# Performance work log

Hardware: AMD Instinct MI355X
Metric: run time of the kernel (lower is better)

## Reference

```python
import jax, jax.numpy as jnp
import numpy as np

N, E, FN, FE, L, G = 4096, 16384, 16, 8, 128, 64
EPS = 1e-5


def setup_inputs() -> dict:
    key = jax.random.key(0)
    ks = iter(jax.random.split(key, 40))

    def lin_w(shape):
        return jax.random.normal(next(ks), shape, jnp.float32) * (1.0 / np.sqrt(shape[0]))

    d = {}
    d["x"] = jax.random.normal(next(ks), (N, FN), jnp.float32)
    d["edge_attr"] = jax.random.normal(next(ks), (E, FE), jnp.float32)
    d["edge_index"] = jax.random.randint(next(ks), (2, E), 0, N)
    d["batch"] = jnp.sort(jax.random.randint(next(ks), (N,), 0, G))
    for i, (cin, cout) in enumerate([(FN, 32), (32, 64), (64, 128)], 1):
        d[f"We{i}"] = lin_w((FE, cin * cout))          # edge_fc weight
        d[f"be{i}"] = jnp.zeros((cin * cout,), jnp.float32)
        d[f"bias{i}"] = jnp.zeros((cout,), jnp.float32)
        d[f"Wr{i}"] = lin_w((cin, cout))               # res_fc weight
        d[f"br{i}"] = jnp.zeros((cout,), jnp.float32)
        d[f"bn_g{i}"] = jnp.ones((cout,), jnp.float32)
        d[f"bn_b{i}"] = jnp.zeros((cout,), jnp.float32)
        d[f"a{i}"] = jnp.float32(0.25)                  # PReLU slope
    d["Wi"] = lin_w((128, 128)); d["bi"] = jnp.zeros((128,), jnp.float32)
    d["Wj"] = lin_w((128, 128)); d["bj"] = jnp.zeros((128,), jnp.float32)
    d["Wfc"] = lin_w((128, 2 * L)); d["bfc"] = jnp.zeros((2 * L,), jnp.float32)
    return d


def _ecc(x, src, dst, norm, edge_attr, We, be, bias, Wr, br, cout, cin):
    # dynamically generated per-edge filter: [E, out, in]
    theta = (edge_attr @ We + be).reshape(E, cout, cin)
    # gather source features, per-edge matvec, degree-normalize (norm_j)
    msg = norm[src][:, None] * jnp.einsum('eoi,ei->eo', theta, x[src])
    # scatter-add into destination nodes + bias + residual linear
    return jax.ops.segment_sum(msg, dst, num_segments=N) + bias + x @ Wr + br


def _bn(x, g, b):
    m = x.mean(0)
    v = x.var(0)  # biased variance, as torch BN training normalization
    return (x - m) * jax.lax.rsqrt(v + EPS) * g + b


def _prelu(x, a):
    return jnp.where(x >= 0, x, a * x)


def reference(x, edge_attr, edge_index, batch,
              We1, be1, bias1, Wr1, br1, bn_g1, bn_b1, a1,
              We2, be2, bias2, Wr2, br2, bn_g2, bn_b2, a2,
              We3, be3, bias3, Wr3, br3, bn_g3, bn_b3, a3,
              Wi, bi, Wj, bj, Wfc, bfc):
    src, dst = edge_index[0], edge_index[1]
    deg = jax.ops.segment_sum(jnp.ones((E,), x.dtype), src, num_segments=N)
    norm = jnp.where(deg > 0, 1.0 / deg, 0.0)

    h = _ecc(x, src, dst, norm, edge_attr, We1, be1, bias1, Wr1, br1, 32, FN)
    h = _prelu(_bn(h, bn_g1, bn_b1), a1)
    h = _ecc(h, src, dst, norm, edge_attr, We2, be2, bias2, Wr2, br2, 64, 32)
    h = _prelu(_bn(h, bn_g2, bn_b2), a2)
    h = _ecc(h, src, dst, norm, edge_attr, We3, be3, bias3, Wr3, br3, 128, 64)
    h = _prelu(_bn(h, bn_g3, bn_b3), a3)

    # gated attention pooling (GGS-NN eq. 7), scatter-sum per graph
    gates = jax.nn.sigmoid(h @ Wi + bi)
    feats = jnp.tanh(h @ Wj + bj)
    pooled = jnp.tanh(jax.ops.segment_sum(gates * feats, batch, num_segments=G))

    z = pooled @ Wfc + bfc  # [G, 2L]
    return z[:, :L], z[:, L:]
```

## Files before the change

### kernel.cpp

```cpp
#include <hip/hip_runtime.h>
#include <math.h>

#define NN 4096
#define NE 16384
#define NG 64

#define OFF_DEG   0
#define OFF_H1    4096
#define OFF_H2    135168
#define OFF_H3    397312
#define OFF_ST1   921600
#define OFF_ST2   921664
#define OFF_ST3   921792
#define OFF_POOL  922048
#define OFF_WC1   930240
#define OFF_WC2   934848
#define OFF_WC3   953280
#define OFF_Y     1027008
#define ZERO_FLOATS 930240

__device__ __forceinline__ void tr_wcat(const float* We, const float* be,
                                        float* Wcat, int CIN, int COUT, int t) {
    int nine = 9 * COUT;
    int i = t / nine; int r = t - i * nine;
    int f = r / COUT; int o = r - f * COUT;
    Wcat[t] = (f < 8) ? We[f * CIN * COUT + o * CIN + i] : be[o * CIN + i];
}

__global__ __launch_bounds__(256) void k_prep(
    const float* __restrict__ We1, const float* __restrict__ be1,
    const float* __restrict__ We2, const float* __restrict__ be2,
    const float* __restrict__ We3, const float* __restrict__ be3,
    const int* __restrict__ ei, float* __restrict__ ws)
{
    int t = blockIdx.x * 256 + threadIdx.x;
    if (t < 4608)  { tr_wcat(We1, be1, ws + OFF_WC1, 16, 32, t); return; }
    t -= 4608;
    if (t < 18432) { tr_wcat(We2, be2, ws + OFF_WC2, 32, 64, t); return; }
    t -= 18432;
    if (t < 73728) { tr_wcat(We3, be3, ws + OFF_WC3, 64, 128, t); return; }
    t -= 73728;
    if (t < NE)    { atomicAdd(&ws[OFF_DEG + ei[t]], 1.0f); }
}

template<int K>
__global__ __launch_bounds__(256) void k_proj(
    const float* __restrict__ A,
    const float* __restrict__ B,
    const float* __restrict__ deg,
    float* __restrict__ Y, int Ncols)
{
    __shared__ float sA[K][68];
    __shared__ float sB[K][68];
    const int tid = threadIdx.x;
    const int m0 = blockIdx.x * 64;
    const int n0 = blockIdx.y * 64;

    for (int t = tid; t < 64 * K; t += 256) {
        int m = t / K, i = t - m * K;
        sA[i][m] = A[(m0 + m) * K + i];
    }
    for (int t = tid; t < 64 * K; t += 256) {
        int i = t / 64, n = t - i * 64;
        int col = n0 + n;
        sB[i][n] = (col < Ncols) ? B[i * Ncols + col] : 0.f;
    }
    __syncthreads();

    const int tn = tid % 16, tm = tid / 16;
    float acc[4][4] = {{0.f}};
#pragma unroll 8
    for (int i = 0; i < K; ++i) {
        float4 a = *(const float4*)&sA[i][tm * 4];
        float4 b = *(const float4*)&sB[i][tn * 4];
        acc[0][0] += a.x * b.x; acc[0][1] += a.x * b.y; acc[0][2] += a.x * b.z; acc[0][3] += a.x * b.w;
        acc[1][0] += a.y * b.x; acc[1][1] += a.y * b.y; acc[1][2] += a.y * b.z; acc[1][3] += a.y * b.w;
        acc[2][0] += a.z * b.x; acc[2][1] += a.z * b.y; acc[2][2] += a.z * b.z; acc[2][3] += a.z * b.w;
        acc[3][0] += a.w * b.x; acc[3][1] += a.w * b.y; acc[3][2] += a.w * b.z; acc[3][3] += a.w * b.w;
    }

#pragma unroll
    for (int mm = 0; mm < 4; ++mm) {
        int m = m0 + tm * 4 + mm;
        float d = deg[m];
        float nrm = d > 0.f ? 1.f / d : 0.f;
#pragma unroll
        for (int nn = 0; nn < 4; ++nn) {
            int col = n0 + tn * 4 + nn;
            if (col < Ncols) Y[(size_t)m * Ncols + col] = acc[mm][nn] * nrm;
        }
    }
}

template<int COUT>
__global__ __launch_bounds__(256) void k_egather(
    const float* __restrict__ Y, const float* __restrict__ eattr,
    const int* __restrict__ ei, float* __restrict__ h)
{
    int idx = blockIdx.x * 256 + threadIdx.x;
    int e = idx / COUT;
    int o = idx - e * COUT;
    int src = ei[e], dst = ei[NE + e];
    const float* y = Y + (size_t)src * (9 * COUT);
    const float* ea = eattr + e * 8;
    float acc = y[8 * COUT + o];
#pragma unroll
    for (int f = 0; f < 8; ++f) acc += ea[f] * y[f * COUT + o];
    atomicAdd(&h[dst * COUT + o], acc);
}

template<int CIN, int COUT, int KN>
__global__ __launch_bounds__(256) void k_node(
    const float* __restrict__ xin, const float* __restrict__ Wr,
    const float* __restrict__ br, const float* __restrict__ bias,
    float* __restrict__ h, float* __restrict__ st)
{
    constexpr int NL = 256 / COUT;
    constexpr int NB = NL * KN;
    constexpr int CINP = CIN | 1;
    __shared__ float sWr[CIN * COUT];
    __shared__ float sX[NB * CINP];
    __shared__ float sred[256];
    const int tid = threadIdx.x;
    const int nbase = blockIdx.x * NB;

    for (int t = tid; t < CIN * COUT; t += 256) sWr[t] = Wr[t];
    for (int t = tid; t < NB * CIN; t += 256) {
        int r = t / CIN, i = t - r * CIN;
        sX[r * CINP + i] = xin[(nbase + r) * CIN + i];
    }
    __syncthreads();

    const int o = tid % COUT;
    const int nl = tid / COUT;
    const float addc = bias[o] + br[o];
    float sum = 0.f, sumsq = 0.f;
    for (int k = 0; k < KN; ++k) {
        int r = nl * KN + k;
        float a = addc;
        for (int i = 0; i < CIN; ++i)
            a += sX[r * CINP + i] * sWr[i * COUT + o];
        int gi = (nbase + r) * COUT + o;
        float hv = h[gi] + a;
        h[gi] = hv;
        sum += hv; sumsq += hv * hv;
    }
    sred[tid] = sum;
    __syncthreads();
    if (tid < COUT) {
        float s = 0.f;
        for (int g2 = 0; g2 < NL; ++g2) s += sred[g2 * COUT + tid];
        atomicAdd(&st[tid], s);
    }
    __syncthreads();
    sred[tid] = sumsq;
    __syncthreads();
    if (tid < COUT) {
        float s = 0.f;
        for (int g2 = 0; g2 < NL; ++g2) s += sred[g2 * COUT + tid];
        atomicAdd(&st[COUT + tid], s);
    }
}

template<int COUT>
__global__ __launch_bounds__(256) void k_bn(
    float* __restrict__ h, const float* __restrict__ st,
    const float* __restrict__ g, const float* __restrict__ b,
    const float* __restrict__ a)
{
    int idx = blockIdx.x * 256 + threadIdx.x;
    int o = idx % COUT;
    float mean = st[o] * (1.f / NN);
    float var = st[COUT + o] * (1.f / NN) - mean * mean;
    var = fmaxf(var, 0.f);
    float inv = rsqrtf(var + 1e-5f);
    float v = (h[idx] - mean) * inv * g[o] + b[o];
    h[idx] = v >= 0.f ? v : a[0] * v;
}

__global__ __launch_bounds__(256) void k_pool(
    const float* __restrict__ h3, const int* __restrict__ batch,
    const float* __restrict__ Wi, const float* __restrict__ bi,
    const float* __restrict__ Wj, const float* __restrict__ bj,
    float* __restrict__ pooled)
{
    constexpr int KN = 8, NB = 16;
    __shared__ float sH[NB * 128];
    __shared__ int sB[NB];
    const int tid = threadIdx.x;
    const int nbase = blockIdx.x * NB;
    for (int t = tid; t < NB * 128; t += 256) sH[t] = h3[nbase * 128 + t];
    if (tid < NB) sB[tid] = batch[nbase + tid];
    __syncthreads();

    const int o = tid % 128, nl = tid / 128;
    float gacc[KN], facc[KN];
#pragma unroll
    for (int k = 0; k < KN; ++k) { gacc[k] = 0.f; facc[k] = 0.f; }
    for (int i = 0; i < 128; ++i) {
        float wi = Wi[i * 128 + o], wj = Wj[i * 128 + o];
#pragma unroll
        for (int k = 0; k < KN; ++k) {
            float hv = sH[(nl * KN + k) * 128 + i];
            gacc[k] += hv * wi;
            facc[k] += hv * wj;
        }
    }
    float bio = bi[o], bjo = bj[o];
#pragma unroll
    for (int k = 0; k < KN; ++k) {
        int r = nl * KN + k;
        float gate = 1.f / (1.f + expf(-(gacc[k] + bio)));
        float feat = tanhf(facc[k] + bjo);
        atomicAdd(&pooled[sB[r] * 128 + o], gate * feat);
    }
}

__global__ __launch_bounds__(256) void k_final(
    const float* __restrict__ pooled, const float* __restrict__ Wfc,
    const float* __restrict__ bfc, float* __restrict__ out)
{
    __shared__ float sP[128];
    const int g = blockIdx.x, c = threadIdx.x;
    if (c < 128) sP[c] = tanhf(pooled[g * 128 + c]);
    __syncthreads();
    float z = bfc[c];
    for (int i = 0; i < 128; ++i) z += sP[i] * Wfc[i * 256 + c];
    int oidx = (c < 128) ? (g * 128 + c) : (NG * 128 + g * 128 + (c - 128));
    out[oidx] = z;
}

extern "C" void kernel_launch(void* const* d_in, const int* in_sizes, int n_in,
                              void* d_out, int out_size, void* d_ws, size_t ws_size,
                              hipStream_t stream)
{
    (void)in_sizes; (void)n_in; (void)out_size; (void)ws_size;
    const float* x     = (const float*)d_in[0];
    const float* eattr = (const float*)d_in[1];
    const int*   ei    = (const int*)d_in[2];
    const int*   batch = (const int*)d_in[3];
    const float* We1 = (const float*)d_in[4];
    const float* be1 = (const float*)d_in[5];
    const float* bias1 = (const float*)d_in[6];
    const float* Wr1 = (const float*)d_in[7];
    const float* br1 = (const float*)d_in[8];
    const float* bg1 = (const float*)d_in[9];
    const float* bb1 = (const float*)d_in[10];
    const float* a1  = (const float*)d_in[11];
    const float* We2 = (const float*)d_in[12];
    const float* be2 = (const float*)d_in[13];
    const float* bias2 = (const float*)d_in[14];
    const float* Wr2 = (const float*)d_in[15];
    const float* br2 = (const float*)d_in[16];
    const float* bg2 = (const float*)d_in[17];
    const float* bb2 = (const float*)d_in[18];
    const float* a2  = (const float*)d_in[19];
    const float* We3 = (const float*)d_in[20];
    const float* be3 = (const float*)d_in[21];
    const float* bias3 = (const float*)d_in[22];
    const float* Wr3 = (const float*)d_in[23];
    const float* br3 = (const float*)d_in[24];
    const float* bg3 = (const float*)d_in[25];
    const float* bb3 = (const float*)d_in[26];
    const float* a3  = (const float*)d_in[27];
    const float* Wi  = (const float*)d_in[28];
    const float* bi  = (const float*)d_in[29];
    const float* Wj  = (const float*)d_in[30];
    const float* bj  = (const float*)d_in[31];
    const float* Wfc = (const float*)d_in[32];
    const float* bfc = (const float*)d_in[33];
    float* ws  = (float*)d_ws;
    float* out = (float*)d_out;

    hipMemsetAsync(d_ws, 0, (size_t)ZERO_FLOATS * sizeof(float), stream);
    k_prep<<<442, 256, 0, stream>>>(We1, be1, We2, be2, We3, be3, ei, ws);

    k_proj<16><<<dim3(64, 5), 256, 0, stream>>>(x, ws + OFF_WC1, ws + OFF_DEG, ws + OFF_Y, 288);
    k_egather<32><<<NE * 32 / 256, 256, 0, stream>>>(ws + OFF_Y, eattr, ei, ws + OFF_H1);
    k_node<16, 32, 8><<<NN / 64, 256, 0, stream>>>(x, Wr1, br1, bias1, ws + OFF_H1, ws + OFF_ST1);
    k_bn<32><<<NN * 32 / 256, 256, 0, stream>>>(ws + OFF_H1, ws + OFF_ST1, bg1, bb1, a1);

    k_proj<32><<<dim3(64, 9), 256, 0, stream>>>(ws + OFF_H1, ws + OFF_WC2, ws + OFF_DEG, ws + OFF_Y, 576);
    k_egather<64><<<NE * 64 / 256, 256, 0, stream>>>(ws + OFF_Y, eattr, ei, ws + OFF_H2);
    k_node<32, 64, 8><<<NN / 32, 256, 0, stream>>>(ws + OFF_H1, Wr2, br2, bias2, ws + OFF_H2, ws + OFF_ST2);
    k_bn<64><<<NN * 64 / 256, 256, 0, stream>>>(ws + OFF_H2, ws + OFF_ST2, bg2, bb2, a2);

    k_proj<64><<<dim3(64, 18), 256, 0, stream>>>(ws + OFF_H2, ws + OFF_WC3, ws + OFF_DEG, ws + OFF_Y, 1152);
    k_egather<128><<<NE * 128 / 256, 256, 0, stream>>>(ws + OFF_Y, eattr, ei, ws + OFF_H3);
    k_node<64, 128, 8><<<NN / 16, 256, 0, stream>>>(ws + OFF_H2, Wr3, br3, bias3, ws + OFF_H3, ws + OFF_ST3);
    k_bn<128><<<NN * 128 / 256, 256, 0, stream>>>(ws + OFF_H3, ws + OFF_ST3, bg3, bb3, a3);

    k_pool<<<NN / 16, 256, 0, stream>>>(ws + OFF_H3, batch, Wi, bi, Wj, bj, ws + OFF_POOL);
    k_final<<<NG, 256, 0, stream>>>(ws + OFF_POOL, Wfc, bfc, out);
}
```

Baseline: 256.4 us.

## Fuse BN+PReLU into consumer kernels, vectorize edge gather, retune node tiling

Drops the three standalone BN/PReLU kernels. Each consumer (the next layer's projection, its residual node kernel, and pooling) now recomputes the per-channel scale and shift from the accumulated stats and applies the affine and PReLU while loading its inputs into shared memory. The edge gather now handles four output channels per thread with float4 loads, cutting thread count and index loads. Node-kernel KN values are reduced for more blocks on the early layers. This removes one launch and a full read/write of h per layer, at the cost of redundant per-block stat computation and an extra barrier.

```diff
diff --git a/kernel.cpp b/kernel.cpp
--- a/kernel.cpp
+++ b/kernel.cpp
@@ -43,22 +43,48 @@
     if (t < NE)    { atomicAdd(&ws[OFF_DEG + ei[t]], 1.0f); }
 }
 
-template<int K>
+template<int K, bool BN>
 __global__ __launch_bounds__(256) void k_proj(
     const float* __restrict__ A,
     const float* __restrict__ B,
     const float* __restrict__ deg,
-    float* __restrict__ Y, int Ncols)
+    float* __restrict__ Y, int Ncols,
+    const float* __restrict__ st, const float* __restrict__ g,
+    const float* __restrict__ b, const float* __restrict__ a)
 {
     __shared__ float sA[K][68];
     __shared__ float sB[K][68];
+    __shared__ float sS[K];
+    __shared__ float sT[K];
+    __shared__ float sAl;
     const int tid = threadIdx.x;
     const int m0 = blockIdx.x * 64;
     const int n0 = blockIdx.y * 64;
 
+    if constexpr (BN) {
+        if (tid < K) {
+            float mean = st[tid] * (1.f / NN);
+            float var  = st[K + tid] * (1.f / NN) - mean * mean;
+            var = fmaxf(var, 0.f);
+            float inv = rsqrtf(var + 1e-5f);
+            float s = inv * g[tid];
+            sS[tid] = s;
+            sT[tid] = b[tid] - mean * s;
+        }
+        if (tid == 0) sAl = a[0];
+    }
+    __syncthreads();
+    float al = 0.f;
+    if constexpr (BN) al = sAl;
+
     for (int t = tid; t < 64 * K; t += 256) {
         int m = t / K, i = t - m * K;
-        sA[i][m] = A[(m0 + m) * K + i];
+        float v = A[(m0 + m) * K + i];
+        if constexpr (BN) {
+            v = fmaf(v, sS[i], sT[i]);
+            v = v >= 0.f ? v : al * v;
+        }
+        sA[i][m] = v;
     }
     for (int t = tid; t < 64 * K; t += 256) {
         int i = t / 64, n = t - i * 64;
@@ -71,12 +97,12 @@
     float acc[4][4] = {{0.f}};
 #pragma unroll 8
     for (int i = 0; i < K; ++i) {
-        float4 a = *(const float4*)&sA[i][tm * 4];
-        float4 b = *(const float4*)&sB[i][tn * 4];
-        acc[0][0] += a.x * b.x; acc[0][1] += a.x * b.y; acc[0][2] += a.x * b.z; acc[0][3] += a.x * b.w;
-        acc[1][0] += a.y * b.x; acc[1][1] += a.y * b.y; acc[1][2] += a.y * b.z; acc[1][3] += a.y * b.w;
-        acc[2][0] += a.z * b.x; acc[2][1] += a.z * b.y; acc[2][2] += a.z * b.z; acc[2][3] += a.z * b.w;
-        acc[3][0] += a.w * b.x; acc[3][1] += a.w * b.y; acc[3][2] += a.w * b.z; acc[3][3] += a.w * b.w;
+        float4 av = *(const float4*)&sA[i][tm * 4];
+        float4 bv = *(const float4*)&sB[i][tn * 4];
+        acc[0][0] += av.x * bv.x; acc[0][1] += av.x * bv.y; acc[0][2] += av.x * bv.z; acc[0][3] += av.x * bv.w;
+        acc[1][0] += av.y * bv.x; acc[1][1] += av.y * bv.y; acc[1][2] += av.y * bv.z; acc[1][3] += av.y * bv.w;
+        acc[2][0] += av.z * bv.x; acc[2][1] += av.z * bv.y; acc[2][2] += av.z * bv.z; acc[2][3] += av.z * bv.w;
+        acc[3][0] += av.w * bv.x; acc[3][1] += av.w * bv.y; acc[3][2] += av.w * bv.z; acc[3][3] += av.w * bv.w;
     }
 
 #pragma unroll
@@ -97,23 +123,39 @@
     const float* __restrict__ Y, const float* __restrict__ eattr,
     const int* __restrict__ ei, float* __restrict__ h)
 {
+    constexpr int TPE = COUT / 4;
     int idx = blockIdx.x * 256 + threadIdx.x;
-    int e = idx / COUT;
-    int o = idx - e * COUT;
+    int e = idx / TPE;
+    int q = idx - e * TPE;
     int src = ei[e], dst = ei[NE + e];
-    const float* y = Y + (size_t)src * (9 * COUT);
-    const float* ea = eattr + e * 8;
-    float acc = y[8 * COUT + o];
-#pragma unroll
-    for (int f = 0; f < 8; ++f) acc += ea[f] * y[f * COUT + o];
-    atomicAdd(&h[dst * COUT + o], acc);
-}
-
-template<int CIN, int COUT, int KN>
+    const float4* y4 = (const float4*)(Y + (size_t)src * (9 * COUT));
+    const float4* ea4 = (const float4*)(eattr + e * 8);
+    float4 ea0 = ea4[0], ea1 = ea4[1];
+    float4 acc = y4[8 * TPE + q];
+#define FMA4(s, v) { float4 _t = (v); acc.x += (s)*_t.x; acc.y += (s)*_t.y; acc.z += (s)*_t.z; acc.w += (s)*_t.w; }
+    FMA4(ea0.x, y4[0 * TPE + q]);
+    FMA4(ea0.y, y4[1 * TPE + q]);
+    FMA4(ea0.z, y4[2 * TPE + q]);
+    FMA4(ea0.w, y4[3 * TPE + q]);
+    FMA4(ea1.x, y4[4 * TPE + q]);
+    FMA4(ea1.y, y4[5 * TPE + q]);
+    FMA4(ea1.z, y4[6 * TPE + q]);
+    FMA4(ea1.w, y4[7 * TPE + q]);
+#undef FMA4
+    float* hp = h + (size_t)dst * COUT + 4 * q;
+    atomicAdd(hp + 0, acc.x);
+    atomicAdd(hp + 1, acc.y);
+    atomicAdd(hp + 2, acc.z);
+    atomicAdd(hp + 3, acc.w);
+}
+
+template<int CIN, int COUT, int KN, bool BN>
 __global__ __launch_bounds__(256) void k_node(
     const float* __restrict__ xin, const float* __restrict__ Wr,
     const float* __restrict__ br, const float* __restrict__ bias,
-    float* __restrict__ h, float* __restrict__ st)
+    float* __restrict__ h, float* __restrict__ st_out,
+    const float* __restrict__ st_in, const float* __restrict__ g,
+    const float* __restrict__ b, const float* __restrict__ a)
 {
     constexpr int NL = 256 / COUT;
     constexpr int NB = NL * KN;
@@ -121,13 +163,37 @@
     __shared__ float sWr[CIN * COUT];
     __shared__ float sX[NB * CINP];
     __shared__ float sred[256];
+    __shared__ float sS[CIN];
+    __shared__ float sT[CIN];
+    __shared__ float sAl;
     const int tid = threadIdx.x;
     const int nbase = blockIdx.x * NB;
 
+    if constexpr (BN) {
+        if (tid < CIN) {
+            float mean = st_in[tid] * (1.f / NN);
+            float var  = st_in[CIN + tid] * (1.f / NN) - mean * mean;
+            var = fmaxf(var, 0.f);
+            float inv = rsqrtf(var + 1e-5f);
+            float s = inv * g[tid];
+            sS[tid] = s;
+            sT[tid] = b[tid] - mean * s;
+        }
+        if (tid == 0) sAl = a[0];
+    }
     for (int t = tid; t < CIN * COUT; t += 256) sWr[t] = Wr[t];
+    __syncthreads();
+    float al = 0.f;
+    if constexpr (BN) al = sAl;
+
     for (int t = tid; t < NB * CIN; t += 256) {
         int r = t / CIN, i = t - r * CIN;
-        sX[r * CINP + i] = xin[(nbase + r) * CIN + i];
+        float v = xin[(nbase + r) * CIN + i];
+        if constexpr (BN) {
+            v = fmaf(v, sS[i], sT[i]);
+            v = v >= 0.f ? v : al * v;
+        }
+        sX[r * CINP + i] = v;
     }
     __syncthreads();
 
@@ -137,11 +203,11 @@
     float sum = 0.f, sumsq = 0.f;
     for (int k = 0; k < KN; ++k) {
         int r = nl * KN + k;
-        float a = addc;
+        float acc = addc;
         for (int i = 0; i < CIN; ++i)
-            a += sX[r * CINP + i] * sWr[i * COUT + o];
+            acc += sX[r * CINP + i] * sWr[i * COUT + o];
         int gi = (nbase + r) * COUT + o;
-        float hv = h[gi] + a;
+        float hv = h[gi] + acc;
         h[gi] = hv;
         sum += hv; sumsq += hv * hv;
     }
@@ -150,7 +216,7 @@
     if (tid < COUT) {
         float s = 0.f;
         for (int g2 = 0; g2 < NL; ++g2) s += sred[g2 * COUT + tid];
-        atomicAdd(&st[tid], s);
+        atomicAdd(&st_out[tid], s);
     }
     __syncthreads();
     sred[tid] = sumsq;
@@ -158,38 +224,47 @@
     if (tid < COUT) {
         float s = 0.f;
         for (int g2 = 0; g2 < NL; ++g2) s += sred[g2 * COUT + tid];
-        atomicAdd(&st[COUT + tid], s);
-    }
-}
-
-template<int COUT>
-__global__ __launch_bounds__(256) void k_bn(
-    float* __restrict__ h, const float* __restrict__ st,
-    const float* __restrict__ g, const float* __restrict__ b,
-    const float* __restrict__ a)
-{
-    int idx = blockIdx.x * 256 + threadIdx.x;
-    int o = idx % COUT;
-    float mean = st[o] * (1.f / NN);
-    float var = st[COUT + o] * (1.f / NN) - mean * mean;
-    var = fmaxf(var, 0.f);
-    float inv = rsqrtf(var + 1e-5f);
-    float v = (h[idx] - mean) * inv * g[o] + b[o];
-    h[idx] = v >= 0.f ? v : a[0] * v;
+        atomicAdd(&st_out[COUT + tid], s);
+    }
 }
 
 __global__ __launch_bounds__(256) void k_pool(
     const float* __restrict__ h3, const int* __restrict__ batch,
     const float* __restrict__ Wi, const float* __restrict__ bi,
     const float* __restrict__ Wj, const float* __restrict__ bj,
-    float* __restrict__ pooled)
+    float* __restrict__ pooled,
+    const float* __restrict__ st, const float* __restrict__ g,
+    const float* __restrict__ b, const float* __restrict__ a)
 {
     constexpr int KN = 8, NB = 16;
     __shared__ float sH[NB * 128];
     __shared__ int sB[NB];
+    __shared__ float sS[128];
+    __shared__ float sT[128];
+    __shared__ float sAl;
     const int tid = threadIdx.x;
     const int nbase = blockIdx.x * NB;
-    for (int t = tid; t < NB * 128; t += 256) sH[t] = h3[nbase * 128 + t];
+
+    if (tid < 128) {
+        float mean = st[tid] * (1.f / NN);
+        float var  = st[128 + tid] * (1.f / NN) - mean * mean;
+        var = fmaxf(var, 0.f);
+        float inv = rsqrtf(var + 1e-5f);
+        float s = inv * g[tid];
+        sS[tid] = s;
+        sT[tid] = b[tid] - mean * s;
+    }
+    if (tid == 0) sAl = a[0];
+    __syncthreads();
+    const float al = sAl;
+
+    for (int t = tid; t < NB * 128; t += 256) {
+        int c = t & 127;
+        float v = h3[nbase * 128 + t];
+        v = fmaf(v, sS[c], sT[c]);
+        v = v >= 0.f ? v : al * v;
+        sH[t] = v;
+    }
     if (tid < NB) sB[tid] = batch[nbase + tid];
     __syncthreads();
 
@@ -275,21 +350,31 @@
     hipMemsetAsync(d_ws, 0, (size_t)ZERO_FLOATS * sizeof(float), stream);
     k_prep<<<442, 256, 0, stream>>>(We1, be1, We2, be2, We3, be3, ei, ws);
 
-    k_proj<16><<<dim3(64, 5), 256, 0, stream>>>(x, ws + OFF_WC1, ws + OFF_DEG, ws + OFF_Y, 288);
-    k_egather<32><<<NE * 32 / 256, 256, 0, stream>>>(ws + OFF_Y, eattr, ei, ws + OFF_H1);
-    k_node<16, 32, 8><<<NN / 64, 256, 0, stream>>>(x, Wr1, br1, bias1, ws + OFF_H1, ws + OFF_ST1);
-    k_bn<32><<<NN * 32 / 256, 256, 0, stream>>>(ws + OFF_H1, ws + OFF_ST1, bg1, bb1, a1);
-
-    k_proj<32><<<dim3(64, 9), 256, 0, stream>>>(ws + OFF_H1, ws + OFF_WC2, ws + OFF_DEG, ws + OFF_Y, 576);
-    k_egather<64><<<NE * 64 / 256, 256, 0, stream>>>(ws + OFF_Y, eattr, ei, ws + OFF_H2);
-    k_node<32, 64, 8><<<NN / 32, 256, 0, stream>>>(ws + OFF_H1, Wr2, br2, bias2, ws + OFF_H2, ws + OFF_ST2);
-    k_bn<64><<<NN * 64 / 256, 256, 0, stream>>>(ws + OFF_H2, ws + OFF_ST2, bg2, bb2, a2);
-
-    k_proj<64><<<dim3(64, 18), 256, 0, stream>>>(ws + OFF_H2, ws + OFF_WC3, ws + OFF_DEG, ws + OFF_Y, 1152);
-    k_egather<128><<<NE * 128 / 256, 256, 0, stream>>>(ws + OFF_Y, eattr, ei, ws + OFF_H3);
-    k_node<64, 128, 8><<<NN / 16, 256, 0, stream>>>(ws + OFF_H2, Wr3, br3, bias3, ws + OFF_H3, ws + OFF_ST3);
-    k_bn<128><<<NN * 128 / 256, 256, 0, stream>>>(ws + OFF_H3, ws + OFF_ST3, bg3, bb3, a3);
-
-    k_pool<<<NN / 16, 256, 0, stream>>>(ws + OFF_H3, batch, Wi, bi, Wj, bj, ws + OFF_POOL);
+    k_proj<16, false><<<dim3(64, 5), 256, 0, stream>>>(
+        x, ws + OFF_WC1, ws + OFF_DEG, ws + OFF_Y, 288,
+        nullptr, nullptr, nullptr, nullptr);
+    k_egather<32><<<NE * 8 / 256, 256, 0, stream>>>(ws + OFF_Y, eattr, ei, ws + OFF_H1);
+    k_node<16, 32, 2, false><<<NN / 16, 256, 0, stream>>>(
+        x, Wr1, br1, bias1, ws + OFF_H1, ws + OFF_ST1,
+        nullptr, nullptr, nullptr, nullptr);
+
+    k_proj<32, true><<<dim3(64, 9), 256, 0, stream>>>(
+        ws + OFF_H1, ws + OFF_WC2, ws + OFF_DEG, ws + OFF_Y, 576,
+        ws + OFF_ST1, bg1, bb1, a1);
+    k_egather<64><<<NE * 16 / 256, 256, 0, stream>>>(ws + OFF_Y, eattr, ei, ws + OFF_H2);
+    k_node<32, 64, 4, true><<<NN / 16, 256, 0, stream>>>(
+        ws + OFF_H1, Wr2, br2, bias2, ws + OFF_H2, ws + OFF_ST2,
+        ws + OFF_ST1, bg1, bb1, a1);
+
+    k_proj<64, true><<<dim3(64, 18), 256, 0, stream>>>(
+        ws + OFF_H2, ws + OFF_WC3, ws + OFF_DEG, ws + OFF_Y, 1152,
+        ws + OFF_ST2, bg2, bb2, a2);
+    k_egather<128><<<NE * 32 / 256, 256, 0, stream>>>(ws + OFF_Y, eattr, ei, ws + OFF_H3);
+    k_node<64, 128, 8, true><<<NN / 16, 256, 0, stream>>>(
+        ws + OFF_H2, Wr3, br3, bias3, ws + OFF_H3, ws + OFF_ST3,
+        ws + OFF_ST2, bg2, bb2, a2);
+
+    k_pool<<<NN / 16, 256, 0, stream>>>(ws + OFF_H3, batch, Wi, bi, Wj, bj, ws + OFF_POOL,
+                                        ws + OFF_ST3, bg3, bb3, a3);
     k_final<<<NG, 256, 0, stream>>>(ws + OFF_POOL, Wfc, bfc, out);
 }
```

Measured after the change: 295.5 us. 15.2% more time.
